# Performance work log

Hardware: AMD Instinct MI355X
Metric: run time of the kernel (lower is better)

## Reference

```python
import jax, jax.numpy as jnp
import numpy as np
import math

B, S, SENC, D, H, FF, V = 4, 512, 512, 1024, 16, 4096, 50257
MAX_HOP = 6          # n_layers -> max ACT hops
THRESH = 1.0 - 0.01  # ACT halting threshold
EPS = 1e-12          # LAYER_NORM_EPS
NEG = -1e20          # neginf for fp32 masking
DH = D // H


def _sincos(n_pos, dim):
    # create_position_codes: sin on even dims, cos on odd dims
    pos = np.arange(n_pos, dtype=np.float64)[:, None]
    j = np.arange(dim // 2, dtype=np.float64)[None, :]
    ang = pos / np.power(10000.0, 2.0 * j / dim)
    out = np.zeros((n_pos, dim), dtype=np.float32)
    out[:, 0::2] = np.sin(ang)
    out[:, 1::2] = np.cos(ang)
    return jnp.asarray(out)


def setup_inputs() -> dict:
    key = jax.random.key(0)
    ks = jax.random.split(key, 20)
    def lin_w(k, fan_in, fan_out):
        return (jax.random.normal(k, (fan_in, fan_out), jnp.float32)
                * (1.0 / math.sqrt(fan_in)))
    inp = {
        "tokens": jax.random.randint(ks[0], (B, S), 0, V),
        "encoder_output": jax.random.normal(ks[1], (B, SENC, D), jnp.float32),
        "encoder_mask": jnp.ones((B, SENC), jnp.int32),
        "emb": jax.random.normal(ks[2], (V, D), jnp.float32) * 0.02,
        "sa_qw": lin_w(ks[3], D, D), "sa_qb": jnp.zeros((D,), jnp.float32),
        "sa_kw": lin_w(ks[4], D, D), "sa_kb": jnp.zeros((D,), jnp.float32),
        "sa_vw": lin_w(ks[5], D, D), "sa_vb": jnp.zeros((D,), jnp.float32),
        "sa_ow": lin_w(ks[6], D, D), "sa_ob": jnp.zeros((D,), jnp.float32),
        "ca_qw": lin_w(ks[7], D, D), "ca_qb": jnp.zeros((D,), jnp.float32),
        "ca_kw": lin_w(ks[8], D, D), "ca_kb": jnp.zeros((D,), jnp.float32),
        "ca_vw": lin_w(ks[9], D, D), "ca_vb": jnp.zeros((D,), jnp.float32),
        "ca_ow": lin_w(ks[10], D, D), "ca_ob": jnp.zeros((D,), jnp.float32),
        "ln1_g": jnp.ones((D,), jnp.float32), "ln1_b": jnp.zeros((D,), jnp.float32),
        "ln2_g": jnp.ones((D,), jnp.float32), "ln2_b": jnp.zeros((D,), jnp.float32),
        "ln3_g": jnp.ones((D,), jnp.float32), "ln3_b": jnp.zeros((D,), jnp.float32),
        "ff_w1": lin_w(ks[11], D, FF), "ff_b1": jnp.zeros((FF,), jnp.float32),
        "ff_w2": lin_w(ks[12], FF, D), "ff_b2": jnp.zeros((D,), jnp.float32),
        "act_w": jax.random.normal(ks[13], (D,), jnp.float32) * 0.02,
        "act_b": jnp.ones((), jnp.float32),  # p.bias.data.fill_(1)
    }
    return inp


def _ln(x, g, b):
    m = x.mean(-1, keepdims=True)
    v = ((x - m) ** 2).mean(-1, keepdims=True)
    return (x - m) / jnp.sqrt(v + EPS) * g + b


def _mha(x, kv, maskb, qw, qb, kw, kb, vw, vb, ow, ob):
    Bq, Sq, _ = x.shape
    Sk = kv.shape[1]
    q = (x @ qw + qb).reshape(Bq, Sq, H, DH).transpose(0, 2, 1, 3) / math.sqrt(DH)
    k = (kv @ kw + kb).reshape(Bq, Sk, H, DH).transpose(0, 2, 1, 3)
    v = (kv @ vw + vb).reshape(Bq, Sk, H, DH).transpose(0, 2, 1, 3)
    sc = jnp.einsum('bhqd,bhkd->bhqk', q, k)
    sc = jnp.where(maskb, sc, NEG)
    a = jax.nn.softmax(sc, axis=-1)
    o = jnp.einsum('bhqk,bhkd->bhqd', a, v).transpose(0, 2, 1, 3).reshape(Bq, Sq, D)
    return o @ ow + ob


def reference(tokens, encoder_output, encoder_mask, emb,
              sa_qw, sa_qb, sa_kw, sa_kb, sa_vw, sa_vb, sa_ow, sa_ob,
              ca_qw, ca_qb, ca_kw, ca_kb, ca_vw, ca_vb, ca_ow, ca_ob,
              ln1_g, ln1_b, ln2_g, ln2_b, ln3_g, ln3_b,
              ff_w1, ff_b1, ff_w2, ff_b2, act_w, act_b):
    pos_codes = _sincos(S, D)       # [S, D]
    time_codes = _sincos(MAX_HOP, D)  # [MAX_HOP, D]
    x = emb[tokens] * math.sqrt(D)  # embeddings_scale
    dec_mask = jnp.tril(jnp.ones((S, S), bool))[None, None]          # causal
    enc_maskb = (encoder_mask != 0)[:, None, None, :]                # [B,1,1,Senc]

    def layer(t):
        r = t
        t = _mha(t, t, dec_mask, sa_qw, sa_qb, sa_kw, sa_kb, sa_vw, sa_vb, sa_ow, sa_ob)
        t = _ln(t + r, ln1_g, ln1_b)
        r = t
        t = _mha(t, encoder_output, enc_maskb, ca_qw, ca_qb, ca_kw, ca_kb, ca_vw, ca_vb, ca_ow, ca_ob)
        t = _ln(t + r, ln2_g, ln2_b)
        r = t
        t = jax.nn.relu(t @ ff_w1 + ff_b1) @ ff_w2 + ff_b2
        return _ln(t + r, ln3_g, ln3_b)

    def step(carry, t_idx):
        tensor, prev, hp, rem, nup = carry
        tensor = tensor + pos_codes[None] + time_codes[t_idx][None, None]
        p = jax.nn.sigmoid(tensor @ act_w + act_b)                   # [B,S]
        still = (hp < 1.0).astype(jnp.float32)
        cond = hp + p * still
        new_halted = (cond > THRESH).astype(jnp.float32) * still
        still = (cond <= THRESH).astype(jnp.float32) * still
        hp = hp + p * still
        rem = rem + new_halted * (1.0 - hp)
        hp = hp + new_halted * rem
        nup = nup + still + new_halted
        uw = (p * still + new_halted * rem)[..., None]
        tensor = layer(tensor)
        prev = tensor * uw + prev * (1.0 - uw)
        return (tensor, prev, hp, rem, nup), None

    z = jnp.zeros((B, S), jnp.float32)
    init = (x, jnp.zeros_like(x), z, z, z)
    # Running all MAX_HOP steps is exactly equivalent to the torch while-loop:
    # after a position halts, its update weight is 0 and state is frozen.
    (_, prev, hp, rem, nup), _ = jax.lax.scan(step, init, jnp.arange(MAX_HOP))
    return prev
```

## Files before the change

kernel.cpp:

```cpp
#include <hip/hip_runtime.h>
#include <math.h>

#define BB 4
#define SS 512
#define SE 512
#define DD 1024
#define HH 16
#define FFD 4096
#define NHOP 6

typedef float f32x4 __attribute__((ext_vector_type(4)));
typedef _Float16 h8 __attribute__((ext_vector_type(8)));
typedef _Float16 h4 __attribute__((ext_vector_type(4)));

#define GLD16(gp, lp)                                                     \
  __builtin_amdgcn_global_load_lds(                                       \
      (const __attribute__((address_space(1))) void*)(gp),                \
      (__attribute__((address_space(3))) void*)(lp), 16, 0, 0)

template <int N>
__device__ __forceinline__ void vwait() {
  if constexpr (N == 0) asm volatile("s_waitcnt vmcnt(0)" ::: "memory");
  else if constexpr (N == 8) asm volatile("s_waitcnt vmcnt(8)" ::: "memory");
}

__device__ __forceinline__ float blockSum256(float v, float* s4) {
#pragma unroll
  for (int m = 32; m >= 1; m >>= 1) v += __shfl_xor(v, m);
  __syncthreads();
  if ((threadIdx.x & 63) == 0) s4[threadIdx.x >> 6] = v;
  __syncthreads();
  return s4[0] + s4[1] + s4[2] + s4[3];
}

__device__ __forceinline__ void split16(float v, _Float16& h, _Float16& l) {
  h = (_Float16)v;
  l = (_Float16)(v - (float)h);
}

__device__ __forceinline__ int swzel(int row, int slot) {
  return (row << 6) + ((slot ^ (row & 7)) << 3);
}

__global__ void sincos_kernel(float* __restrict__ out, int n) {
  for (int i = blockIdx.x * blockDim.x + threadIdx.x; i < n;
       i += gridDim.x * blockDim.x) {
    int p = i >> 10, d = i & 1023, j = d >> 1;
    double ang = (double)p / pow(10000.0, (2.0 * j) / 1024.0);
    out[i] = (float)((d & 1) ? cos(ang) : sin(ang));
  }
}

__global__ void embed_kernel(const int* __restrict__ tok,
                             const float* __restrict__ emb,
                             float* __restrict__ out, int n) {
  for (int i = blockIdx.x * blockDim.x + threadIdx.x; i < n;
       i += gridDim.x * blockDim.x) {
    int row = i >> 10, d = i & 1023;
    out[i] = emb[(size_t)tok[row] * DD + d] * 32.0f;
  }
}

__global__ void asplit_kernel(const float* __restrict__ x,
                              _Float16* __restrict__ h,
                              _Float16* __restrict__ l, int n) {
  for (int i = blockIdx.x * blockDim.x + threadIdx.x; i < n;
       i += gridDim.x * blockDim.x)
    split16(x[i], h[i], l[i]);
}

__global__ __launch_bounds__(256)
void actcodes_kernel(const float* __restrict__ ten, const float* __restrict__ pos,
                     const float* __restrict__ tim, int hop,
                     const float* __restrict__ aw, const float* __restrict__ ab,
                     float* __restrict__ hp, float* __restrict__ rem,
                     float* __restrict__ uw, _Float16* __restrict__ th,
                     _Float16* __restrict__ tl) {
  __shared__ float s4[4];
  int row = blockIdx.x;
  int srow = row & 511;
  size_t base = (size_t)row * DD;
  float s = 0.f;
#pragma unroll
  for (int k = 0; k < 4; ++k) {
    int d = threadIdx.x + k * 256;
    float v = ten[base + d] + pos[(srow << 10) + d] + tim[(hop << 10) + d];
    split16(v, th[base + d], tl[base + d]);
    s += v * aw[d];
  }
  float z = blockSum256(s, s4);
  if (threadIdx.x == 0) {
    z += ab[0];
    float p = 1.0f / (1.0f + expf(-z));
    float h = hp[row], rm = rem[row];
    float s0 = (h < 1.0f) ? 1.0f : 0.0f;
    float cond = h + p * s0;
    float nh = (cond > 0.99f) ? s0 : 0.0f;
    float s1 = (cond <= 0.99f) ? s0 : 0.0f;
    h = h + p * s1;
    rm = rm + nh * (1.0f - h);
    h = h + nh * rm;
    hp[row] = h;
    rem[row] = rm;
    uw[row] = p * s1 + nh * rm;
  }
}

__global__ __launch_bounds__(256)
void lnres_kernel(const float* __restrict__ a, const _Float16* __restrict__ rh,
                  const _Float16* __restrict__ rl, const float* __restrict__ g,
                  const float* __restrict__ be, float* __restrict__ outf,
                  _Float16* __restrict__ oh, _Float16* __restrict__ ol,
                  const float* __restrict__ uwv, float* __restrict__ po,
                  int mode) {
  __shared__ float s4[4];
  int row = blockIdx.x;
  size_t base = (size_t)row * DD;
  float x[4];
#pragma unroll
  for (int k = 0; k < 4; ++k) {
    size_t idx = base + threadIdx.x + k * 256;
    x[k] = a[idx] + ((float)rh[idx] + (float)rl[idx]);
  }
  float mean = blockSum256(x[0] + x[1] + x[2] + x[3], s4) * (1.0f / 1024.0f);
  float q = 0.f;
#pragma unroll
  for (int k = 0; k < 4; ++k) {
    float dv = x[k] - mean;
    q += dv * dv;
  }
  float var = blockSum256(q, s4) * (1.0f / 1024.0f);
  float inv = 1.0f / sqrtf(var + 1e-12f);
  float u = (mode == 0) ? uwv[row] : 0.f;
#pragma unroll
  for (int k = 0; k < 4; ++k) {
    int d = threadIdx.x + k * 256;
    size_t idx = base + d;
    float y = (x[k] - mean) * inv * g[d] + be[d];
    if (mode == 0) {
      outf[idx] = y;
      po[idx] = y * u + po[idx] * (1.0f - u);
    } else {
      split16(y, oh[idx], ol[idx]);
    }
  }
}

__global__ __launch_bounds__(256)
void wsplit_kernel(const float* __restrict__ W, _Float16* __restrict__ WhT,
                   _Float16* __restrict__ WlT, int K, int N) {
  __shared__ float t[32][33];
  int k0 = blockIdx.y << 5, n0 = blockIdx.x << 5;
  int c = threadIdx.x & 31, r8 = threadIdx.x >> 5;
  for (int rr = r8; rr < 32; rr += 8)
    t[rr][c] = W[(size_t)(k0 + rr) * N + n0 + c];
  __syncthreads();
  for (int rr = r8; rr < 32; rr += 8) {
    float v = t[c][rr];
    split16(v, WhT[(size_t)(n0 + rr) * K + k0 + c],
            WlT[(size_t)(n0 + rr) * K + k0 + c]);
  }
}

__global__ void concat3_kernel(const float* __restrict__ a,
                               const float* __restrict__ b,
                               const float* __restrict__ c,
                               float* __restrict__ o) {
  int i = blockIdx.x * 256 + threadIdx.x;
  if (i < 3072) o[i] = (i < 1024) ? a[i] : ((i < 2048) ? b[i - 1024] : c[i - 2048]);
}

template <int EPI>
__global__ __launch_bounds__(256) void gemm_pl(
    const _Float16* __restrict__ Ah, const _Float16* __restrict__ Al,
    const _Float16* __restrict__ Bh, const _Float16* __restrict__ Bl,
    const float* __restrict__ bias, float* __restrict__ Cf,
    _Float16* __restrict__ Ch, _Float16* __restrict__ Cl,
    _Float16* __restrict__ Ch2, _Float16* __restrict__ Cl2,
    _Float16* __restrict__ Ch3, _Float16* __restrict__ Cl3, int M, int N,
    int K, float scale) {
  __shared__ __align__(16) _Float16 sA0[2][4096], sA1[2][4096];
  __shared__ __align__(16) _Float16 sB0[2][4096], sB1[2][4096];
  const int tid = threadIdx.x;
  const int lane = tid & 63, wid = tid >> 6;
  const int wr = wid >> 1, wc = wid & 1;
  int bx = blockIdx.x, by = blockIdx.y;
  {
    int nb = gridDim.x * gridDim.y;
    if ((nb & 7) == 0) {
      int flat = by * gridDim.x + bx;
      int swz = (flat & 7) * (nb >> 3) + (flat >> 3);
      bx = swz % gridDim.x;
      by = swz / gridDim.x;
    }
  }
  const int m0 = by << 6, n0 = bx << 6;
  const int l15 = lane & 15, l4 = lane >> 4;

  f32x4 acc[2][2];
#pragma unroll
  for (int i = 0; i < 2; ++i)
#pragma unroll
    for (int j = 0; j < 2; ++j) acc[i][j] = (f32x4){0.f, 0.f, 0.f, 0.f};

  auto STAGE = [&](int kt, int buf) {
    const int ko = kt << 6;
#pragma unroll
    for (int c = 0; c < 2; ++c) {
      int idx = (c << 8) + tid;
      int row = idx >> 3, gs = (idx & 7) ^ (row & 7);
      int de = (c << 11) + (wid << 9);
      size_t ga = (size_t)(m0 + row) * K + ko + (gs << 3);
      GLD16(Ah + ga, &sA0[buf][de]);
      GLD16(Al + ga, &sA1[buf][de]);
      size_t gb = (size_t)(n0 + row) * K + ko + (gs << 3);
      GLD16(Bh + gb, &sB0[buf][de]);
      GLD16(Bl + gb, &sB1[buf][de]);
    }
  };

  const int nk = K >> 6;
  STAGE(0, 0);
  int cur = 0;
  for (int kt = 0; kt < nk; ++kt) {
    if (kt + 1 < nk) {
      STAGE(kt + 1, cur ^ 1);
      vwait<8>();
    } else {
      vwait<0>();
    }
    __builtin_amdgcn_s_barrier();
    __builtin_amdgcn_sched_barrier(0);
    const _Float16* pA0 = sA0[cur];
    const _Float16* pA1 = sA1[cur];
    const _Float16* pB0 = sB0[cur];
    const _Float16* pB1 = sB1[cur];
#pragma unroll
    for (int ks = 0; ks < 2; ++ks) {
      h8 a0[2], a1[2], b0[2], b1[2];
#pragma unroll
      for (int f = 0; f < 2; ++f) {
        int m = (wr << 5) + (f << 4) + l15;
        int so = swzel(m, (ks << 2) + l4);
        a0[f] = *(const h8*)&pA0[so];
        a1[f] = *(const h8*)&pA1[so];
        int n = (wc << 5) + (f << 4) + l15;
        int sn = swzel(n, (ks << 2) + l4);
        b0[f] = *(const h8*)&pB0[sn];
        b1[f] = *(const h8*)&pB1[sn];
      }
#pragma unroll
      for (int fi = 0; fi < 2; ++fi)
#pragma unroll
        for (int fj = 0; fj < 2; ++fj) {
          acc[fi][fj] = __builtin_amdgcn_mfma_f32_16x16x32_f16(
              a0[fi], b0[fj], acc[fi][fj], 0, 0, 0);
          acc[fi][fj] = __builtin_amdgcn_mfma_f32_16x16x32_f16(
              a1[fi], b0[fj], acc[fi][fj], 0, 0, 0);
          acc[fi][fj] = __builtin_amdgcn_mfma_f32_16x16x32_f16(
              a0[fi], b1[fj], acc[fi][fj], 0, 0, 0);
        }
    }
    __builtin_amdgcn_sched_barrier(0);
    __builtin_amdgcn_s_barrier();
    cur ^= 1;
  }
#pragma unroll
  for (int fi = 0; fi < 2; ++fi) {
    int row = m0 + (wr << 5) + (fi << 4) + (l4 << 2);
#pragma unroll
    for (int fj = 0; fj < 2; ++fj) {
      int col = n0 + (wc << 5) + (fj << 4) + l15;
      float bz = bias[col];
      float ov[4];
#pragma unroll
      for (int r = 0; r < 4; ++r) ov[r] = acc[fi][fj][r] + bz;
      if (EPI == 0) {
#pragma unroll
        for (int r = 0; r < 4; ++r) Cf[(size_t)(row + r) * N + col] = ov[r];
      } else if (EPI == 1) {
#pragma unroll
        for (int r = 0; r < 4; ++r) {
          float o = fmaxf(ov[r], 0.f);
          size_t idx = (size_t)(row + r) * N + col;
          split16(o, Ch[idx], Cl[idx]);
        }
      } else if (EPI == 3) {
        int b = row >> 9, h = col >> 6, d = col & 63;
#pragma unroll
        for (int r = 0; r < 4; ++r) {
          int sr = (row + r) & 511;
          size_t q = ((size_t)(b * HH + h) * SS + sr) * 64 + d;
          split16(ov[r] * scale, Ch[q], Cl[q]);
        }
      } else if (EPI == 4) {
        int b = row >> 9, s0 = row & 511, h = col >> 6, d = col & 63;
        h4 hv, lv;
#pragma unroll
        for (int r = 0; r < 4; ++r) {
          _Float16 hh, ll;
          split16(ov[r], hh, ll);
          hv[r] = hh;
          lv[r] = ll;
        }
        size_t vo = ((size_t)(b * HH + h) * 64 + d) * SS + s0;
        *(h4*)&Ch[vo] = hv;
        *(h4*)&Cl[vo] = lv;
      } else {
        int reg = col >> 10;
        int c = col & 1023;
        int b = row >> 9, h = c >> 6, d = c & 63;
        if (reg == 2) {
          int s0 = row & 511;
          h4 hv, lv;
#pragma unroll
          for (int r = 0; r < 4; ++r) {
            _Float16 hh, ll;
            split16(ov[r], hh, ll);
            hv[r] = hh;
            lv[r] = ll;
          }
          size_t vo = ((size_t)(b * HH + h) * 64 + d) * SS + s0;
          *(h4*)&Ch3[vo] = hv;
          *(h4*)&Cl3[vo] = lv;
        } else {
#pragma unroll
          for (int r = 0; r < 4; ++r) {
            float o = (reg == 0) ? ov[r] * scale : ov[r];
            int sr = (row + r) & 511;
            size_t q = ((size_t)(b * HH + h) * SS + sr) * 64 + d;
            if (reg == 0) split16(o, Ch[q], Cl[q]);
            else split16(o, Ch2[q], Cl2[q]);
          }
        }
      }
    }
  }
}

template <int CAUSAL>
__global__ __launch_bounds__(256) void flash_mfma(
    const _Float16* __restrict__ Qph, const _Float16* __restrict__ Qpl,
    const _Float16* __restrict__ Kph, const _Float16* __restrict__ Kpl,
    const _Float16* __restrict__ Vph, const _Float16* __restrict__ Vpl,
    _Float16* __restrict__ AOh, _Float16* __restrict__ AOl,
    const int* __restrict__ mask, int Sk) {
  __shared__ __align__(16) _Float16 sKh[2][4096], sKl[2][4096];
  __shared__ __align__(16) _Float16 sVh[2][4096], sVl[2][4096];
  __shared__ __align__(16) _Float16 sPh[4096], sPl[4096];
  const int tid = threadIdx.x, lane = tid & 63, wid = tid >> 6;
  const int l15 = lane & 15, l4 = lane >> 4;
  const int flat = blockIdx.x;
  const int bh = flat >> 3, b = bh >> 4;
  int qt = flat & 7;
  if (CAUSAL && (flat >> 8)) qt = 7 - qt;
  const size_t qkb = (size_t)bh * SS * 64;
  const size_t vtb = (size_t)bh * 64 * Sk;

  int srow[2], slg[2], sde[2];
#pragma unroll
  for (int c = 0; c < 2; ++c) {
    int u = (c << 8) + tid;
    srow[c] = u >> 3;
    slg[c] = (u & 7) ^ (srow[c] & 7);
    sde[c] = (c << 11) + (wid << 9);
  }

  unsigned mbits = 0xFFFFFFFFu;
  if (!CAUSAL && mask != nullptr) {
    mbits = 0u;
#pragma unroll
    for (int kt = 0; kt < 8; ++kt)
#pragma unroll
      for (int fj = 0; fj < 4; ++fj)
        mbits |= (mask[b * Sk + kt * 64 + fj * 16 + l15] != 0 ? 1u : 0u)
                 << (kt * 4 + fj);
  }

  h8 aqh[2], aql[2];
#pragma unroll
  for (int ks = 0; ks < 2; ++ks) {
    size_t qa = qkb + (size_t)(qt * 64 + wid * 16 + l15) * 64 + ks * 32 + l4 * 8;
    aqh[ks] = *(const h8*)(Qph + qa);
    aql[ks] = *(const h8*)(Qpl + qa);
  }
  f32x4 o_[4];
  float m_[4], l_[4];
#pragma unroll
  for (int i = 0; i < 4; ++i) o_[i] = (f32x4){0.f, 0.f, 0.f, 0.f};
#pragma unroll
  for (int r = 0; r < 4; ++r) { m_[r] = -3.0e38f; l_[r] = 0.f; }

  auto STAGE = [&](int kt, int buf) {
#pragma unroll
    for (int c = 0; c < 2; ++c) {
      size_t ksrc = qkb + (size_t)(kt * 64 + srow[c]) * 64 + slg[c] * 8;
      size_t vsrc = vtb + (size_t)srow[c] * Sk + kt * 64 + slg[c] * 8;
      GLD16(Kph + ksrc, &sKh[buf][sde[c]]);
      GLD16(Kpl + ksrc, &sKl[buf][sde[c]]);
      GLD16(Vph + vsrc, &sVh[buf][sde[c]]);
      GLD16(Vpl + vsrc, &sVl[buf][sde[c]]);
    }
  };

  const int nkt = CAUSAL ? (qt + 1) : (Sk >> 6);
  STAGE(0, 0);
  int cur = 0;
  for (int kt = 0; kt < nkt; ++kt) {
    if (kt + 1 < nkt) {
      STAGE(kt + 1, cur ^ 1);
      vwait<8>();
    } else {
      vwait<0>();
    }
    __builtin_amdgcn_s_barrier();
    __builtin_amdgcn_sched_barrier(0);
    const _Float16* pKh = sKh[cur];
    const _Float16* pKl = sKl[cur];
    const _Float16* pVh = sVh[cur];
    const _Float16* pVl = sVl[cur];
    f32x4 sc[4];
#pragma unroll
    for (int fj = 0; fj < 4; ++fj) {
      sc[fj] = (f32x4){0.f, 0.f, 0.f, 0.f};
#pragma unroll
      for (int ks = 0; ks < 2; ++ks) {
        int off = swzel(fj * 16 + l15, ks * 4 + l4);
        h8 bkh = *(const h8*)&pKh[off];
        h8 bkl = *(const h8*)&pKl[off];
        sc[fj] = __builtin_amdgcn_mfma_f32_16x16x32_f16(aqh[ks], bkh, sc[fj], 0, 0, 0);
        sc[fj] = __builtin_amdgcn_mfma_f32_16x16x32_f16(aql[ks], bkh, sc[fj], 0, 0, 0);
        sc[fj] = __builtin_amdgcn_mfma_f32_16x16x32_f16(aqh[ks], bkl, sc[fj], 0, 0, 0);
      }
    }
    if (CAUSAL && kt == qt) {
#pragma unroll
      for (int fj = 0; fj < 4; ++fj)
#pragma unroll
        for (int r = 0; r < 4; ++r)
          if (fj * 16 + l15 > wid * 16 + l4 * 4 + r) sc[fj][r] = -1e20f;
    }
    if (!CAUSAL) {
#pragma unroll
      for (int fj = 0; fj < 4; ++fj)
        if (!((mbits >> (kt * 4 + fj)) & 1u)) {
#pragma unroll
          for (int r = 0; r < 4; ++r) sc[fj][r] = -1e20f;
        }
    }
#pragma unroll
    for (int r = 0; r < 4; ++r) {
      float rm = fmaxf(fmaxf(sc[0][r], sc[1][r]), fmaxf(sc[2][r], sc[3][r]));
#pragma unroll
      for (int mk = 1; mk < 16; mk <<= 1) rm = fmaxf(rm, __shfl_xor(rm, mk));
      float mn = fmaxf(m_[r], rm);
      float f = __expf(m_[r] - mn);
      float rs = 0.f;
      int prow = wid * 16 + l4 * 4 + r;
#pragma unroll
      for (int fj = 0; fj < 4; ++fj) {
        float p = __expf(sc[fj][r] - mn);
        rs += p;
        int col = fj * 16 + l15;
        int el = (prow << 6) + ((((col >> 3) ^ (prow & 7))) << 3) + (col & 7);
        _Float16 ph = (_Float16)p;
        sPh[el] = ph;
        sPl[el] = (_Float16)(p - (float)ph);
      }
#pragma unroll
      for (int mk = 1; mk < 16; mk <<= 1) rs += __shfl_xor(rs, mk);
      l_[r] = l_[r] * f + rs;
      m_[r] = mn;
#pragma unroll
      for (int df = 0; df < 4; ++df) o_[df][r] *= f;
    }
#pragma unroll
    for (int ks = 0; ks < 2; ++ks) {
      int poff = swzel(wid * 16 + l15, ks * 4 + l4);
      h8 aph = *(const h8*)&sPh[poff];
      h8 apl = *(const h8*)&sPl[poff];
#pragma unroll
      for (int df = 0; df < 4; ++df) {
        int voff = swzel(df * 16 + l15, ks * 4 + l4);
        h8 bvh = *(const h8*)&pVh[voff];
        h8 bvl = *(const h8*)&pVl[voff];
        o_[df] = __builtin_amdgcn_mfma_f32_16x16x32_f16(aph, bvh, o_[df], 0, 0, 0);
        o_[df] = __builtin_amdgcn_mfma_f32_16x16x32_f16(apl, bvh, o_[df], 0, 0, 0);
        o_[df] = __builtin_amdgcn_mfma_f32_16x16x32_f16(aph, bvl, o_[df], 0, 0, 0);
      }
    }
    __builtin_amdgcn_sched_barrier(0);
    __builtin_amdgcn_s_barrier();
    cur ^= 1;
  }
#pragma unroll
  for (int r = 0; r < 4; ++r) {
    float inv = 1.0f / l_[r];
    int row = qt * 64 + wid * 16 + l4 * 4 + r;
    size_t ob = ((size_t)b * SS + row) * DD + (bh & 15) * 64;
#pragma unroll
    for (int df = 0; df < 4; ++df) {
      float o = o_[df][r] * inv;
      split16(o, AOh[ob + df * 16 + l15], AOl[ob + df * 16 + l15]);
    }
  }
}

extern "C" void kernel_launch(void* const* d_in, const int* in_sizes, int n_in,
                              void* d_out, int out_size, void* d_ws,
                              size_t ws_size, hipStream_t stream) {
  const int* tokens = (const int*)d_in[0];
  const float* enc = (const float*)d_in[1];
  const int* encmask = (const int*)d_in[2];
  const float* emb = (const float*)d_in[3];
  const float* sa_qw = (const float*)d_in[4];
  const float* sa_qb = (const float*)d_in[5];
  const float* sa_kw = (const float*)d_in[6];
  const float* sa_kb = (const float*)d_in[7];
  const float* sa_vw = (const float*)d_in[8];
  const float* sa_vb = (const float*)d_in[9];
  const float* sa_ow = (const float*)d_in[10];
  const float* sa_ob = (const float*)d_in[11];
  const float* ca_qw = (const float*)d_in[12];
  const float* ca_qb = (const float*)d_in[13];
  const float* ca_kw = (const float*)d_in[14];
  const float* ca_kb = (const float*)d_in[15];
  const float* ca_vw = (const float*)d_in[16];
  const float* ca_vb = (const float*)d_in[17];
  const float* ca_ow = (const float*)d_in[18];
  const float* ca_ob = (const float*)d_in[19];
  const float* ln1_g = (const float*)d_in[20];
  const float* ln1_b = (const float*)d_in[21];
  const float* ln2_g = (const float*)d_in[22];
  const float* ln2_b = (const float*)d_in[23];
  const float* ln3_g = (const float*)d_in[24];
  const float* ln3_b = (const float*)d_in[25];
  const float* ff_w1 = (const float*)d_in[26];
  const float* ff_b1 = (const float*)d_in[27];
  const float* ff_w2 = (const float*)d_in[28];
  const float* ff_b2 = (const float*)d_in[29];
  const float* act_w = (const float*)d_in[30];
  const float* act_b = (const float*)d_in[31];
  float* out = (float*)d_out;

  const size_t nbsd = (size_t)BB * SS * DD;
  const size_t nff = (size_t)BB * SS * FFD;
  const size_t nbs = (size_t)BB * SS;
  const size_t wsm = (size_t)DD * DD;
  const size_t wff = (size_t)DD * FFD;

  float* w = (float*)d_ws;
  float* POS = w;  w += (size_t)SS * DD;
  float* TIM = w;  w += (size_t)NHOP * DD;
  float* TEN = w;  w += nbsd;
  float* PR = w;   w += nbsd;
  float* T2R = w;  w += (size_t)2048 * 3072;
  float* QKVB = w; w += 3072;
  float* HPp = w;  w += nbs;
  float* REMp = w; w += nbs;
  float* UWp = w;  w += nbs;
  _Float16* hp16 = (_Float16*)w;
  auto halloc = [&](size_t n) { _Float16* r = hp16; hp16 += n; return r; };
  _Float16* TINh = halloc(nbsd); _Float16* TINl = halloc(nbsd);
  _Float16* AOh = halloc(nbsd);  _Float16* AOl = halloc(nbsd);
  _Float16* FFHh = halloc(nff);  _Float16* FFHl = halloc(nff);
  _Float16* qkvWh = halloc(3 * wsm); _Float16* qkvWl = halloc(3 * wsm);
  _Float16* saoWh = halloc(wsm); _Float16* saoWl = halloc(wsm);
  _Float16* caqWh = halloc(wsm); _Float16* caqWl = halloc(wsm);
  _Float16* caoWh = halloc(wsm); _Float16* caoWl = halloc(wsm);
  _Float16* ff1Wh = halloc(wff); _Float16* ff1Wl = halloc(wff);
  _Float16* ff2Wh = halloc(wff); _Float16* ff2Wl = halloc(wff);
  _Float16* EKh = halloc(nbsd); _Float16* EKl = halloc(nbsd);
  _Float16* EVh = halloc(nbsd); _Float16* EVl = halloc(nbsd);
  size_t need = (size_t)((char*)hp16 - (char*)d_ws);
  if (ws_size < need) return;

  _Float16* T3h = TINh; _Float16* T3l = TINl;
  _Float16* T2h = (_Float16*)T2R;
  _Float16* T2l = (_Float16*)T2R + nbsd;
  _Float16* Qph = FFHh;             _Float16* Qpl = FFHh + nbsd;
  _Float16* Kph = FFHh + 2 * nbsd;  _Float16* Kpl = FFHh + 3 * nbsd;
  _Float16* Vph = FFHl;             _Float16* Vpl = FFHl + nbsd;
  _Float16* CQh = FFHl + 2 * nbsd;  _Float16* CQl = FFHl + 3 * nbsd;

  hipMemsetAsync(d_out, 0, nbsd * sizeof(float), stream);
  hipMemsetAsync(HPp, 0, 2 * nbs * sizeof(float), stream);
  sincos_kernel<<<dim3(512), dim3(256), 0, stream>>>(POS, SS * DD);
  sincos_kernel<<<dim3(24), dim3(256), 0, stream>>>(TIM, NHOP * DD);
  embed_kernel<<<dim3(2048), dim3(256), 0, stream>>>(tokens, emb, TEN, (int)nbsd);
  asplit_kernel<<<dim3(2048), dim3(256), 0, stream>>>(enc, TINh, TINl, (int)nbsd);

  auto wsplit = [&](const float* W, _Float16* h, _Float16* l, int K, int N) {
    wsplit_kernel<<<dim3(N >> 5, K >> 5), dim3(256), 0, stream>>>(W, h, l, K, N);
  };
  wsplit(sa_qw, qkvWh, qkvWl, DD, DD);
  wsplit(sa_kw, qkvWh + wsm, qkvWl + wsm, DD, DD);
  wsplit(sa_vw, qkvWh + 2 * wsm, qkvWl + 2 * wsm, DD, DD);
  wsplit(sa_ow, saoWh, saoWl, DD, DD);
  wsplit(ca_qw, caqWh, caqWl, DD, DD);
  wsplit(ca_kw, FFHh, FFHh + wsm, DD, DD);
  wsplit(ca_vw, FFHh + 2 * wsm, FFHh + 3 * wsm, DD, DD);
  wsplit(ca_ow, caoWh, caoWl, DD, DD);
  wsplit(ff_w1, ff1Wh, ff1Wl, DD, FFD);
  wsplit(ff_w2, ff2Wh, ff2Wl, FFD, DD);
  concat3_kernel<<<dim3(12), dim3(256), 0, stream>>>(sa_qb, sa_kb, sa_vb, QKVB);

  auto gemmF = [&](const _Float16* ah, const _Float16* al, const _Float16* bh,
                   const _Float16* bl, const float* bi, float* cf, int M, int N,
                   int K) {
    gemm_pl<0><<<dim3(N / 64, M / 64), dim3(256), 0, stream>>>(
        ah, al, bh, bl, bi, cf, nullptr, nullptr, nullptr, nullptr, nullptr,
        nullptr, M, N, K, 1.f);
  };

  gemm_pl<3><<<dim3(16, 32), dim3(256), 0, stream>>>(
      TINh, TINl, FFHh, FFHh + wsm, ca_kb, nullptr, EKh, EKl, nullptr, nullptr,
      nullptr, nullptr, 2048, DD, DD, 1.f);
  gemm_pl<4><<<dim3(16, 32), dim3(256), 0, stream>>>(
      TINh, TINl, FFHh + 2 * wsm, FFHh + 3 * wsm, ca_vb, nullptr, EVh, EVl,
      nullptr, nullptr, nullptr, nullptr, 2048, DD, DD, 1.f);

  for (int t = 0; t < NHOP; ++t) {
    actcodes_kernel<<<dim3(2048), dim3(256), 0, stream>>>(
        TEN, POS, TIM, t, act_w, act_b, HPp, REMp, UWp, TINh, TINl);
    gemm_pl<2><<<dim3(48, 32), dim3(256), 0, stream>>>(
        TINh, TINl, qkvWh, qkvWl, QKVB, nullptr, Qph, Qpl, Kph, Kpl, Vph, Vpl,
        2048, 3072, DD, 0.125f);
    flash_mfma<1><<<dim3(512), dim3(256), 0, stream>>>(
        Qph, Qpl, Kph, Kpl, Vph, Vpl, AOh, AOl, nullptr, SS);
    gemmF(AOh, AOl, saoWh, saoWl, sa_ob, PR, 2048, DD, DD);
    lnres_kernel<<<dim3(2048), dim3(256), 0, stream>>>(
        PR, TINh, TINl, ln1_g, ln1_b, nullptr, T2h, T2l, nullptr, nullptr, 1);
    gemm_pl<3><<<dim3(16, 32), dim3(256), 0, stream>>>(
        T2h, T2l, caqWh, caqWl, ca_qb, nullptr, CQh, CQl, nullptr, nullptr,
        nullptr, nullptr, 2048, DD, DD, 0.125f);
    flash_mfma<0><<<dim3(512), dim3(256), 0, stream>>>(
        CQh, CQl, EKh, EKl, EVh, EVl, AOh, AOl, encmask, SE);
    gemmF(AOh, AOl, caoWh, caoWl, ca_ob, PR, 2048, DD, DD);
    lnres_kernel<<<dim3(2048), dim3(256), 0, stream>>>(
        PR, T2h, T2l, ln2_g, ln2_b, nullptr, T3h, T3l, nullptr, nullptr, 1);
    gemm_pl<1><<<dim3(64, 32), dim3(256), 0, stream>>>(
        T3h, T3l, ff1Wh, ff1Wl, ff_b1, nullptr, FFHh, FFHl, nullptr, nullptr,
        nullptr, nullptr, 2048, FFD, DD, 1.f);
    gemmF(FFHh, FFHl, ff2Wh, ff2Wl, ff_b2, PR, 2048, DD, FFD);
    lnres_kernel<<<dim3(2048), dim3(256), 0, stream>>>(
        PR, T3h, T3l, ln3_g, ln3_b, TEN, nullptr, nullptr, UWp, out, 0);
  }
}
```

Before: 2.165 ms.

## Add 128x64-tile split-fp16 GEMM for QKV and FF1 projections

```diff
diff --git a/kernel.cpp b/kernel.cpp
--- a/kernel.cpp
+++ b/kernel.cpp
@@ -21,6 +21,7 @@
 template <int N>
 __device__ __forceinline__ void vwait() {
   if constexpr (N == 0) asm volatile("s_waitcnt vmcnt(0)" ::: "memory");
+  else if constexpr (N == 6) asm volatile("s_waitcnt vmcnt(6)" ::: "memory");
   else if constexpr (N == 8) asm volatile("s_waitcnt vmcnt(8)" ::: "memory");
 }
 
@@ -306,6 +307,134 @@
         size_t vo = ((size_t)(b * HH + h) * 64 + d) * SS + s0;
         *(h4*)&Ch[vo] = hv;
         *(h4*)&Cl[vo] = lv;
+      }
+    }
+  }
+}
+
+template <int EPI>
+__global__ __launch_bounds__(256) void gemm_big(
+    const _Float16* __restrict__ Ah, const _Float16* __restrict__ Al,
+    const _Float16* __restrict__ Bh, const _Float16* __restrict__ Bl,
+    const float* __restrict__ bias, _Float16* __restrict__ Ch,
+    _Float16* __restrict__ Cl, _Float16* __restrict__ Ch2,
+    _Float16* __restrict__ Cl2, _Float16* __restrict__ Ch3,
+    _Float16* __restrict__ Cl3, int M, int N, int K, float scale) {
+  constexpr int FM = 4, FN = 2;
+  constexpr int MT = 128, NT = 64;
+  constexpr int SA = 2, SB = 1;
+  constexpr int L = 2 * (SA + SB);
+  __shared__ __align__(16) _Float16 sA0[2][MT * 32], sA1[2][MT * 32];
+  __shared__ __align__(16) _Float16 sB0[2][NT * 32], sB1[2][NT * 32];
+  const int tid = threadIdx.x;
+  const int lane = tid & 63, wid = tid >> 6;
+  const int wr = wid >> 1, wc = wid & 1;
+  int bx = blockIdx.x, by = blockIdx.y;
+  {
+    int nb = gridDim.x * gridDim.y;
+    if ((nb & 7) == 0) {
+      int flat = by * gridDim.x + bx;
+      int swz = (flat & 7) * (nb >> 3) + (flat >> 3);
+      bx = swz % gridDim.x;
+      by = swz / gridDim.x;
+    }
+  }
+  const int m0 = by * MT, n0 = bx * NT;
+  const int l15 = lane & 15, l4 = lane >> 4;
+
+  f32x4 acc[FM][FN];
+#pragma unroll
+  for (int i = 0; i < FM; ++i)
+#pragma unroll
+    for (int j = 0; j < FN; ++j) acc[i][j] = (f32x4){0.f, 0.f, 0.f, 0.f};
+
+  auto STAGE = [&](int kt, int buf) {
+    const int ko = kt << 5;
+#pragma unroll
+    for (int c = 0; c < SA; ++c) {
+      int slot = tid + (c << 8);
+      int row = slot >> 2, sl = slot & 3;
+      int of = ((sl ^ ((row >> 1) & 3)) << 3);
+      size_t ga = (size_t)(m0 + row) * K + ko + of;
+      int de = (wid << 9) + (c << 11);
+      GLD16(Ah + ga, &sA0[buf][de]);
+      GLD16(Al + ga, &sA1[buf][de]);
+    }
+#pragma unroll
+    for (int c = 0; c < SB; ++c) {
+      int slot = tid + (c << 8);
+      int row = slot >> 2, sl = slot & 3;
+      int of = ((sl ^ ((row >> 1) & 3)) << 3);
+      size_t gb = (size_t)(n0 + row) * K + ko + of;
+      int de = (wid << 9) + (c << 11);
+      GLD16(Bh + gb, &sB0[buf][de]);
+      GLD16(Bl + gb, &sB1[buf][de]);
+    }
+  };
+
+  const int nk = K >> 5;
+  STAGE(0, 0);
+  int cur = 0;
+  for (int kt = 0; kt < nk; ++kt) {
+    if (kt + 1 < nk) {
+      STAGE(kt + 1, cur ^ 1);
+      vwait<L>();
+    } else {
+      vwait<0>();
+    }
+    __builtin_amdgcn_s_barrier();
+    __builtin_amdgcn_sched_barrier(0);
+    const _Float16* pA0 = sA0[cur];
+    const _Float16* pA1 = sA1[cur];
+    const _Float16* pB0 = sB0[cur];
+    const _Float16* pB1 = sB1[cur];
+    h8 a0[FM], a1[FM], b0[FN], b1[FN];
+#pragma unroll
+    for (int f = 0; f < FM; ++f) {
+      int m = wr * (FM * 16) + f * 16 + l15;
+      int st = ((l4 ^ ((m >> 1) & 3)) << 3);
+      a0[f] = *(const h8*)&pA0[(m << 5) + st];
+      a1[f] = *(const h8*)&pA1[(m << 5) + st];
+    }
+#pragma unroll
+    for (int f = 0; f < FN; ++f) {
+      int n = wc * (FN * 16) + f * 16 + l15;
+      int sn = ((l4 ^ ((n >> 1) & 3)) << 3);
+      b0[f] = *(const h8*)&pB0[(n << 5) + sn];
+      b1[f] = *(const h8*)&pB1[(n << 5) + sn];
+    }
+#pragma unroll
+    for (int fi = 0; fi < FM; ++fi)
+#pragma unroll
+      for (int fj = 0; fj < FN; ++fj) {
+        acc[fi][fj] = __builtin_amdgcn_mfma_f32_16x16x32_f16(
+            a0[fi], b0[fj], acc[fi][fj], 0, 0, 0);
+        acc[fi][fj] = __builtin_amdgcn_mfma_f32_16x16x32_f16(
+            a1[fi], b0[fj], acc[fi][fj], 0, 0, 0);
+        acc[fi][fj] = __builtin_amdgcn_mfma_f32_16x16x32_f16(
+            a0[fi], b1[fj], acc[fi][fj], 0, 0, 0);
+      }
+    __builtin_amdgcn_sched_barrier(0);
+    __builtin_amdgcn_s_barrier();
+    cur ^= 1;
+  }
+#pragma unroll
+  for (int fi = 0; fi < FM; ++fi) {
+    int row = m0 + wr * (FM * 16) + fi * 16 + (l4 << 2);
+#pragma unroll
+    for (int fj = 0; fj < FN; ++fj) {
+      int col = n0 + wc * (FN * 16) + fj * 16 + l15;
+      float bz = bias[col];
+      float ov[4];
+#pragma unroll
+      for (int r = 0; r < 4; ++r) ov[r] = acc[fi][fj][r] + bz;
+      if (EPI == 1) {
+#pragma unroll
+        for (int r = 0; r < 4; ++r) {
+          float o = fmaxf(ov[r], 0.f);
+          size_t idx = (size_t)(row + r) * N + col;
+          split16(o, Ch[idx], Cl[idx]);
+        }
       } else {
         int reg = col >> 10;
         int c = col & 1023;
@@ -623,9 +752,9 @@
   for (int t = 0; t < NHOP; ++t) {
     actcodes_kernel<<<dim3(2048), dim3(256), 0, stream>>>(
         TEN, POS, TIM, t, act_w, act_b, HPp, REMp, UWp, TINh, TINl);
-    gemm_pl<2><<<dim3(48, 32), dim3(256), 0, stream>>>(
-        TINh, TINl, qkvWh, qkvWl, QKVB, nullptr, Qph, Qpl, Kph, Kpl, Vph, Vpl,
-        2048, 3072, DD, 0.125f);
+    gemm_big<2><<<dim3(48, 16), dim3(256), 0, stream>>>(
+        TINh, TINl, qkvWh, qkvWl, QKVB, Qph, Qpl, Kph, Kpl, Vph, Vpl, 2048,
+        3072, DD, 0.125f);
     flash_mfma<1><<<dim3(512), dim3(256), 0, stream>>>(
         Qph, Qpl, Kph, Kpl, Vph, Vpl, AOh, AOl, nullptr, SS);
     gemmF(AOh, AOl, saoWh, saoWl, sa_ob, PR, 2048, DD, DD);
@@ -639,9 +768,9 @@
     gemmF(AOh, AOl, caoWh, caoWl, ca_ob, PR, 2048, DD, DD);
     lnres_kernel<<<dim3(2048), dim3(256), 0, stream>>>(
         PR, T2h, T2l, ln2_g, ln2_b, nullptr, T3h, T3l, nullptr, nullptr, 1);
-    gemm_pl<1><<<dim3(64, 32), dim3(256), 0, stream>>>(
-        T3h, T3l, ff1Wh, ff1Wl, ff_b1, nullptr, FFHh, FFHl, nullptr, nullptr,
-        nullptr, nullptr, 2048, FFD, DD, 1.f);
+    gemm_big<1><<<dim3(64, 16), dim3(256), 0, stream>>>(
+        T3h, T3l, ff1Wh, ff1Wl, ff_b1, FFHh, FFHl, nullptr, nullptr, nullptr,
+        nullptr, 2048, FFD, DD, 1.f);
     gemmF(FFHh, FFHl, ff2Wh, ff2Wl, ff_b2, PR, 2048, DD, FFD);
     lnres_kernel<<<dim3(2048), dim3(256), 0, stream>>>(
         PR, T3h, T3l, ln3_g, ln3_b, TEN, nullptr, nullptr, UWp, out, 0);
```

Result: faster. 2.059 ms (-4.9%).
